# Kernel optimization log

Hardware: AMD Instinct MI355X
Metric: run time of the kernel (lower is better)

The kernel has to match this reference:

```python
import jax, jax.numpy as jnp
import numpy as np

B = 1; S = 2048; HID = 1024; NH = 8; HD = 128; INTER = 4096
EPS = 1e-6; THETA = 10000.0


def rms_norm(x, w):
    # Gemma RMSNorm: x * rsqrt(mean(x^2)+eps) * (1 + w)
    v = jnp.mean(x * x, axis=-1, keepdims=True)
    return x * jax.lax.rsqrt(v + EPS) * (1.0 + w)


def rope_cos_sin(seqlen):
    inv = 1.0 / (THETA ** (jnp.arange(0, HD, 2, dtype=jnp.float32) / HD))
    t = jnp.arange(seqlen, dtype=jnp.float32)
    f = jnp.outer(t, inv)                       # (S, HD/2)
    emb = jnp.concatenate([f, f], axis=-1)      # (S, HD)
    return jnp.cos(emb), jnp.sin(emb)


def rotate_half(x):
    x1, x2 = jnp.split(x, 2, axis=-1)
    return jnp.concatenate([-x2, x1], axis=-1)


def apply_rope(x, cos, sin):
    return x * cos[None, None] + rotate_half(x) * sin[None, None]


def expert_forward(x, mask, params):
    """One GemmaDecoderLayer; returns output plus PRE-RoPE q/k/v (as the torch module exposes)."""
    w_ln, wq, wk, wv, wo, w_pln, wg, wu, wd = params
    res = x
    h = rms_norm(x, w_ln)

    def proj(w):
        return (h @ w).reshape(B, -1, NH, HD).transpose(0, 2, 1, 3)  # (B,H,S,D)

    q, k, v = proj(wq), proj(wk), proj(wv)      # stored before rotary in the original
    cos, sin = rope_cos_sin(x.shape[1])
    qr, kr = apply_rope(q, cos, sin), apply_rope(k, cos, sin)
    scores = jnp.einsum('bhqd,bhkd->bhqk', qr, kr) * (HD ** -0.5) + mask
    attn = jnp.einsum('bhqk,bhkd->bhqd', jax.nn.softmax(scores, axis=-1), v)
    attn = attn.transpose(0, 2, 1, 3).reshape(B, -1, NH * HD) @ wo
    h1 = res + attn
    m = rms_norm(h1, w_pln)
    mlp = (jax.nn.gelu(m @ wg, approximate=True) * (m @ wu)) @ wd  # gelu_pytorch_tanh
    return h1 + mlp, q, k, v


def setup_inputs() -> dict:
    key = jax.random.key(0)
    ks = iter(jax.random.split(key, 40))

    def w(shape, scale=0.02):
        return jax.random.normal(next(ks), shape, jnp.float32) * scale

    inp = {
        'x_a': jax.random.normal(next(ks), (B, S, HID), jnp.float32),
        'x_b': jax.random.normal(next(ks), (B, S, HID), jnp.float32),
    }
    tri = jnp.tril(jnp.ones((S, S), bool))
    causal = jnp.where(tri, 0.0, -1e9).astype(jnp.float32)[None, None]  # additive causal mask
    inp['mask_a'] = causal
    inp['mask_b'] = causal
    inp['mix_mask'] = jnp.zeros((B, 1, 2 * S, 2 * S), jnp.float32)      # non-causal cross-expert
    for e in ('a', 'b'):
        inp['w_ln_' + e] = jnp.zeros((HID,), jnp.float32)
        inp['w_q_' + e] = w((HID, NH * HD))
        inp['w_k_' + e] = w((HID, NH * HD))
        inp['w_v_' + e] = w((HID, NH * HD))
        inp['w_o_' + e] = w((NH * HD, HID))
        inp['w_pln_' + e] = jnp.zeros((HID,), jnp.float32)
        inp['w_g_' + e] = w((HID, INTER))
        inp['w_u_' + e] = w((HID, INTER))
        inp['w_d_' + e] = w((INTER, HID))
    return inp


def reference(x_a, x_b, mask_a, mask_b, mix_mask,
              w_ln_a, w_q_a, w_k_a, w_v_a, w_o_a, w_pln_a, w_g_a, w_u_a, w_d_a,
              w_ln_b, w_q_b, w_k_b, w_v_b, w_o_b, w_pln_b, w_g_b, w_u_b, w_d_b):
    pa = (w_ln_a, w_q_a, w_k_a, w_v_a, w_o_a, w_pln_a, w_g_a, w_u_a, w_d_a)
    pb = (w_ln_b, w_q_b, w_k_b, w_v_b, w_o_b, w_pln_b, w_g_b, w_u_b, w_d_b)
    out_a, qa, ka, va = expert_forward(x_a, mask_a, pa)
    out_b, qb, kb, vb = expert_forward(x_b, mask_b, pb)
    # cross-expert mixed attention over concatenated (pre-RoPE) streams
    q = jnp.concatenate([qa, qb], axis=2)
    k = jnp.concatenate([ka, kb], axis=2)
    v = jnp.concatenate([va, vb], axis=2)
    scores = jnp.einsum('bhqd,bhkd->bhqk', q, k) * (HD ** -0.5) + mix_mask
    mixed = jnp.einsum('bhqk,bhkd->bhqd', jax.nn.softmax(scores, axis=-1), v)
    mixed = mixed.transpose(0, 2, 1, 3).reshape(B, 2 * S, NH * HD)
    ma, mb = mixed[:, :S], mixed[:, S:]
    return jnp.stack([out_a + ma @ w_o_a, out_b + mb @ w_o_b])
```

## Files before the change

kernel.cpp:

```cpp
#include <hip/hip_runtime.h>
#include <hip/hip_bf16.h>
#include <math.h>

#define S 2048
#define HID 1024
#define NH 8
#define HD 128
#define INTER 4096
#define EPSV 1e-6f
#define THETA 10000.0f

typedef __hip_bfloat16 bf16;
typedef unsigned short u16;
typedef __attribute__((ext_vector_type(8))) short bf16x8;
typedef __attribute__((ext_vector_type(4))) float f32x4;

__device__ inline float bu2f(u16 u) {
    unsigned int x = ((unsigned int)u) << 16;
    return __uint_as_float(x);
}
__device__ inline u16 f2bu(float f) {
    bf16 h = __float2bfloat16(f);
    return *reinterpret_cast<u16*>(&h);
}
__device__ inline float ldin(const void* p, size_t i, bool isbf) {
    return isbf ? bu2f(((const u16*)p)[i]) : ((const float*)p)[i];
}
__device__ inline float gelu_tanh(float x) {
    float x3 = x * x * x;
    return 0.5f * x * (1.f + tanhf(0.7978845608028654f * (x + 0.044715f * x3)));
}
__device__ inline void gload16(const u16* g, u16* l) {
    __builtin_amdgcn_global_load_lds(
        (const __attribute__((address_space(1))) void*)g,
        (__attribute__((address_space(3))) void*)l, 16, 0, 0);
}

__global__ __launch_bounds__(256) void probe_kernel(const unsigned short* __restrict__ x,
                                                    int* __restrict__ flag) {
    __shared__ int red[256];
    int tid = threadIdx.x;
    int cnt = 0;
    for (int i = tid; i < 2048; i += 256) {
        unsigned short u = x[2 * i];
        int e = (u >> 7) & 0xFF;
        cnt += (e >= 110 && e <= 135) ? 1 : 0;
    }
    red[tid] = cnt;
    __syncthreads();
    for (int off = 128; off > 0; off >>= 1) {
        if (tid < off) red[tid] += red[tid + off];
        __syncthreads();
    }
    if (tid == 0) *flag = (red[0] > 1024) ? 1 : 0;
}

struct TransN {
    const void* W[8];
    u16* T[8];
};
__global__ __launch_bounds__(256) void transpose_wN(TransN tn, const int* __restrict__ flag,
                                                    int K, int N) {
    bool isbf = (*flag != 0);
    const void* W = tn.W[blockIdx.z];
    u16* WT = tn.T[blockIdx.z];
    __shared__ float t[32][33];
    int n0 = blockIdx.x * 32, k0 = blockIdx.y * 32;
    int c = threadIdx.x & 31, r = threadIdx.x >> 5;
#pragma unroll
    for (int p = 0; p < 4; p++)
        t[r + 8 * p][c] = ldin(W, (size_t)(k0 + r + 8 * p) * N + n0 + c, isbf);
    __syncthreads();
#pragma unroll
    for (int p = 0; p < 4; p++) {
        int row = r + 8 * p;
        WT[(size_t)(n0 + row) * K + k0 + c] = f2bu(t[c][row]);
    }
}

__global__ __launch_bounds__(256) void transpose_v(const u16* __restrict__ V0,
                                                   const u16* __restrict__ V1, int sv,
                                                   u16* __restrict__ VT) {
    const u16* V = blockIdx.z ? V1 : V0;
    VT += (size_t)blockIdx.z * ((size_t)NH * HD * S);
    __shared__ u16 t[32][33];
    int k0 = blockIdx.x * 32;
    int d0 = blockIdx.y * 32;
    int c = threadIdx.x & 31, r = threadIdx.x >> 5;
#pragma unroll
    for (int p = 0; p < 4; p++)
        t[r + 8 * p][c] = V[(size_t)(k0 + r + 8 * p) * sv + d0 + c];
    __syncthreads();
#pragma unroll
    for (int p = 0; p < 4; p++)
        VT[(size_t)(d0 + r + 8 * p) * S + k0 + c] = t[c][r + 8 * p];
}

struct RmsDual {
    const void* x[2];
    const void* w[2];
    u16* y[2];
};
__global__ __launch_bounds__(256) void rmsnorm_kernel(RmsDual rd,
                                                      const int* __restrict__ flag,
                                                      int dual) {
    int e = blockIdx.y;
    const void* x = rd.x[e];
    const void* w = rd.w[e];
    u16* y = rd.y[e];
    bool isbf = (*flag != 0);
    bool xbf = dual && isbf;
    int row = blockIdx.x;
    size_t base = (size_t)row * HID;
    __shared__ float red[256];
    float xv[4];
    float s = 0.f;
#pragma unroll
    for (int i = 0; i < 4; i++) {
        float v = ldin(x, base + threadIdx.x + 256 * i, xbf);
        xv[i] = v;
        s += v * v;
    }
    red[threadIdx.x] = s;
    __syncthreads();
    for (int off = 128; off > 0; off >>= 1) {
        if (threadIdx.x < off) red[threadIdx.x] += red[threadIdx.x + off];
        __syncthreads();
    }
    float scale = rsqrtf(red[0] / (float)HID + EPSV);
#pragma unroll
    for (int i = 0; i < 4; i++) {
        int c = threadIdx.x + 256 * i;
        y[base + c] = f2bu(xv[i] * scale * (1.f + ldin(w, c, isbf)));
    }
}

struct GemmDual {
    const u16* A[2];
    const u16* BT[2];
    float* Cf[2];
    u16* Cb[2];
    const void* res[2];
};
template <int BM, int BN, int WRN, int WCN, int EPI>
__global__ __launch_bounds__(256) void gemm_mfma(GemmDual g, const int* __restrict__ flag,
                                                 int M, int N, int K) {
    int eZ = blockIdx.z;
    const u16* __restrict__ A = g.A[eZ];
    const u16* __restrict__ BT = g.BT[eZ];
    float* __restrict__ Cf = g.Cf[eZ];
    u16* __restrict__ Cb = g.Cb[eZ];
    const void* __restrict__ res = g.res[eZ];
    constexpr int BK = 32;
    constexpr int WM = BM / WRN, WN = BN / WCN, TI = WM / 16, TJ = WN / 16;
    __shared__ u16 As[BM * 32];
    __shared__ u16 Bs[BN * 32];
    int tid = threadIdx.x, lane = tid & 63, wv = tid >> 6;
    int wr = wv / WCN, wc = wv % WCN;
    int m = lane & 15, quad = lane >> 4;
    int m0 = blockIdx.y * BM, n0 = blockIdx.x * BN;
    f32x4 acc[TI][TJ] = {};
    for (int k0 = 0; k0 < K; k0 += BK) {
        __syncthreads();
#pragma unroll
        for (int c2 = 0; c2 < BM / 64; c2++) {
            int row0 = (wv * (BM / 64) + c2) * 16;
            int row = row0 + (lane >> 2);
            int ch = lane & 3;
            gload16(&A[(size_t)(m0 + row) * K + k0 + ((ch ^ ((row >> 1) & 3)) << 3)],
                    &As[row0 * 32]);
        }
#pragma unroll
        for (int c2 = 0; c2 < BN / 64; c2++) {
            int row0 = (wv * (BN / 64) + c2) * 16;
            int row = row0 + (lane >> 2);
            int ch = lane & 3;
            gload16(&BT[(size_t)(n0 + row) * K + k0 + ((ch ^ ((row >> 1) & 3)) << 3)],
                    &Bs[row0 * 32]);
        }
        __syncthreads();
        bf16x8 af[TI], bf_[TJ];
#pragma unroll
        for (int i = 0; i < TI; i++) {
            int rr = wr * WM + i * 16 + m;
            af[i] = *reinterpret_cast<const bf16x8*>(&As[rr * 32 + ((quad ^ ((rr >> 1) & 3)) << 3)]);
        }
#pragma unroll
        for (int j = 0; j < TJ; j++) {
            int rr = wc * WN + j * 16 + m;
            bf_[j] = *reinterpret_cast<const bf16x8*>(&Bs[rr * 32 + ((quad ^ ((rr >> 1) & 3)) << 3)]);
        }
#pragma unroll
        for (int i = 0; i < TI; i++)
#pragma unroll
            for (int j = 0; j < TJ; j++)
                acc[i][j] = __builtin_amdgcn_mfma_f32_16x16x32_bf16(af[i], bf_[j], acc[i][j], 0, 0, 0);
    }
    bool isbf = (EPI == 1) ? (*flag != 0) : false;
#pragma unroll
    for (int i = 0; i < TI; i++) {
#pragma unroll
        for (int j = 0; j < TJ; j++) {
#pragma unroll
            for (int r = 0; r < 4; r++) {
                int row = m0 + wr * WM + i * 16 + quad * 4 + r;
                int col = n0 + wc * WN + j * 16 + m;
                size_t idx = (size_t)row * N + col;
                float v = acc[i][j][r];
                if (EPI == 0) Cb[idx] = f2bu(v);
                else if (EPI == 1) Cf[idx] = v + ldin(res, idx, isbf);
                else Cf[idx] = Cf[idx] + v;
            }
        }
    }
}

template <int BM, int BN, int WRN, int WCN>
__global__ __launch_bounds__(256) void gemm_gated_mfma(const u16* __restrict__ A,
                                                       const u16* __restrict__ BgT,
                                                       const u16* __restrict__ BuT,
                                                       u16* __restrict__ C,
                                                       int M, int N, int K) {
    constexpr int BK = 32;
    constexpr int WM = BM / WRN, WN = BN / WCN, TI = WM / 16, TJ = WN / 16;
    __shared__ u16 As[BM * 32];
    __shared__ u16 Bgs[BN * 32];
    __shared__ u16 Bus[BN * 32];
    int tid = threadIdx.x, lane = tid & 63, wv = tid >> 6;
    int wr = wv / WCN, wc = wv % WCN;
    int m = lane & 15, quad = lane >> 4;
    int m0 = blockIdx.y * BM, n0 = blockIdx.x * BN;
    f32x4 accg[TI][TJ] = {};
    f32x4 accu[TI][TJ] = {};
    for (int k0 = 0; k0 < K; k0 += BK) {
        __syncthreads();
#pragma unroll
        for (int c2 = 0; c2 < BM / 64; c2++) {
            int row0 = (wv * (BM / 64) + c2) * 16;
            int row = row0 + (lane >> 2);
            int ch = lane & 3;
            gload16(&A[(size_t)(m0 + row) * K + k0 + ((ch ^ ((row >> 1) & 3)) << 3)],
                    &As[row0 * 32]);
        }
#pragma unroll
        for (int c2 = 0; c2 < BN / 64; c2++) {
            int row0 = (wv * (BN / 64) + c2) * 16;
            int row = row0 + (lane >> 2);
            int ch = lane & 3;
            gload16(&BgT[(size_t)(n0 + row) * K + k0 + ((ch ^ ((row >> 1) & 3)) << 3)],
                    &Bgs[row0 * 32]);
            gload16(&BuT[(size_t)(n0 + row) * K + k0 + ((ch ^ ((row >> 1) & 3)) << 3)],
                    &Bus[row0 * 32]);
        }
        __syncthreads();
        bf16x8 af[TI], bg[TJ], bu[TJ];
#pragma unroll
        for (int i = 0; i < TI; i++) {
            int rr = wr * WM + i * 16 + m;
            af[i] = *reinterpret_cast<const bf16x8*>(&As[rr * 32 + ((quad ^ ((rr >> 1) & 3)) << 3)]);
        }
#pragma unroll
        for (int j = 0; j < TJ; j++) {
            int rr = wc * WN + j * 16 + m;
            int off = rr * 32 + ((quad ^ ((rr >> 1) & 3)) << 3);
            bg[j] = *reinterpret_cast<const bf16x8*>(&Bgs[off]);
            bu[j] = *reinterpret_cast<const bf16x8*>(&Bus[off]);
        }
#pragma unroll
        for (int i = 0; i < TI; i++)
#pragma unroll
            for (int j = 0; j < TJ; j++) {
                accg[i][j] = __builtin_amdgcn_mfma_f32_16x16x32_bf16(af[i], bg[j], accg[i][j], 0, 0, 0);
                accu[i][j] = __builtin_amdgcn_mfma_f32_16x16x32_bf16(af[i], bu[j], accu[i][j], 0, 0, 0);
            }
    }
#pragma unroll
    for (int i = 0; i < TI; i++)
#pragma unroll
        for (int j = 0; j < TJ; j++)
#pragma unroll
            for (int r = 0; r < 4; r++) {
                int row = m0 + wr * WM + i * 16 + quad * 4 + r;
                int col = n0 + wc * WN + j * 16 + m;
                C[(size_t)row * N + col] = f2bu(gelu_tanh(accg[i][j][r]) * accu[i][j][r]);
            }
}

__global__ __launch_bounds__(64) void rope_kernel(const u16* __restrict__ qkv0,
                                                  const u16* __restrict__ qkv1,
                                                  u16* __restrict__ qr,
                                                  u16* __restrict__ kr) {
    const u16* qkv = blockIdx.z ? qkv1 : qkv0;
    size_t zo = (size_t)blockIdx.z * ((size_t)S * HID);
    int b = blockIdx.x;
    int t = b >> 3, h = b & 7;
    int i = threadIdx.x;
    size_t ib = (size_t)t * 3072 + h * HD;
    size_t ob = zo + (size_t)t * HID + h * HD;
    float inv = __expf(-9.210340372f * (float)(2 * i) / (float)HD);
    float f = (float)t * inv;
    float c = cosf(f), s = sinf(f);
    float q1 = bu2f(qkv[ib + i]), q2 = bu2f(qkv[ib + i + 64]);
    qr[ob + i] = f2bu(q1 * c - q2 * s);
    qr[ob + i + 64] = f2bu(q2 * c + q1 * s);
    float k1 = bu2f(qkv[ib + 1024 + i]), k2 = bu2f(qkv[ib + 1024 + i + 64]);
    kr[ob + i] = f2bu(k1 * c - k2 * s);
    kr[ob + i + 64] = f2bu(k2 * c + k1 * s);
}

__device__ inline int swz64(int row, int b) {
    return row * 64 + (b ^ (((row >> 1) & 3) << 4));
}

template <bool CAUSAL>
__global__ __launch_bounds__(256, 2) void attn_mfma_kernel(
    const u16* __restrict__ qa, const u16* __restrict__ qb, int sq,
    const u16* __restrict__ ka, const u16* __restrict__ kb, int sk,
    const u16* __restrict__ vta, const u16* __restrict__ vtb,
    u16* __restrict__ Out, int nkeys) {
    __shared__ char Ks[2][16384];
    __shared__ char VTs[2][16384];

    int tid = threadIdx.x;
    int lane = tid & 63, w = tid >> 6;
    int col = lane & 15, quad = lane >> 4;
    int eZ = CAUSAL ? (int)blockIdx.z : 0;
    int bx = (CAUSAL && eZ) ? ((int)gridDim.x - 1 - (int)blockIdx.x) : (int)blockIdx.x;
    int q0 = bx * 64;
    int h = blockIdx.y;
    const float scale = 0.08838834764831845f;

    int q0r = CAUSAL ? q0 : (q0 & (S - 1));
    const u16* qsel = CAUSAL ? (eZ ? qb : qa) : ((q0 < S) ? qa : qb);
    const u16* qp = qsel + (size_t)q0r * sq;
    bf16x8 aq[4];
#pragma unroll
    for (int t = 0; t < 4; t++)
        aq[t] = *reinterpret_cast<const bf16x8*>(
            qp + (size_t)(16 * w + col) * sq + h * HD + 32 * t + quad * 8);

    const u16* kplo = (CAUSAL && eZ) ? kb : ka;
    const u16* vplo = (CAUSAL && eZ) ? vtb : vta;

    f32x4 o[8] = {};
    float m_ = -1e30f, l_ = 0.f;

    int sA = col + 16 * (2 * (quad & 1));
    int sB = sA + 16;
    bool hi = (quad >> 1) != 0;

    int ntiles = CAUSAL ? (q0 >> 6) + 1 : (nkeys >> 6);

    auto stage = [&](int buf, int tt) {
        int j0r = (tt * 64) & (S - 1);
        bool eb = (!CAUSAL) && (tt >= (S >> 6));
        const u16* kp = eb ? kb : kplo;
        const u16* vp = eb ? vtb : vplo;
        char* kd = &Ks[buf][(tid >> 6) * 1024];
        char* vd = &VTs[buf][(tid >> 6) * 1024];
#pragma unroll
        for (int i = 0; i < 4; i++) {
            int l = 256 * i + tid;
            int key = (l >> 2) & 63;
            int c = (l >> 8) * 4 + ((l & 3) ^ ((key >> 1) & 3));
            gload16(kp + (size_t)(j0r + key) * sk + h * HD + c * 8, (u16*)(kd + i * 4096));
        }
#pragma unroll
        for (int i = 0; i < 4; i++) {
            int l = 256 * i + tid;
            int d = (l >> 2) & 127;
            int c = (l >> 9) * 4 + ((l & 3) ^ ((d >> 1) & 3));
            gload16(vp + (size_t)(h * HD + d) * S + j0r + c * 8, (u16*)(vd + i * 4096));
        }
    };

    stage(0, 0);
    __syncthreads();
    int cur = 0;

    for (int tt = 0; tt < ntiles; tt++) {
        if (tt + 1 < ntiles) stage(cur ^ 1, tt + 1);
        const char* Kb = Ks[cur];
        const char* Vb = VTs[cur];

        f32x4 sc[4] = {};
        __builtin_amdgcn_s_setprio(1);
#pragma unroll
        for (int t = 0; t < 4; t++) {
#pragma unroll
            for (int ct = 0; ct < 4; ct++) {
                bf16x8 kf = *reinterpret_cast<const bf16x8*>(
                    Kb + t * 4096 + swz64(16 * ct + col, quad * 16));
                sc[ct] = __builtin_amdgcn_mfma_f32_16x16x32_bf16(kf, aq[t], sc[ct], 0, 0, 0);
            }
        }
        __builtin_amdgcn_s_setprio(0);
        bool diag = CAUSAL && (tt == ntiles - 1);
#pragma unroll
        for (int ct = 0; ct < 4; ct++) {
#pragma unroll
            for (int r = 0; r < 4; r++) {
                float v = sc[ct][r] * scale;
                if (diag && (16 * ct + 4 * quad + r > 16 * w + col)) v = -1e30f;
                sc[ct][r] = v;
            }
        }

        float mx0 = fmaxf(fmaxf(sc[0][0], sc[0][1]), fmaxf(sc[0][2], sc[0][3]));
        float mx1 = fmaxf(fmaxf(sc[1][0], sc[1][1]), fmaxf(sc[1][2], sc[1][3]));
        float mx2 = fmaxf(fmaxf(sc[2][0], sc[2][1]), fmaxf(sc[2][2], sc[2][3]));
        float mx3 = fmaxf(fmaxf(sc[3][0], sc[3][1]), fmaxf(sc[3][2], sc[3][3]));
        float rmax = fmaxf(fmaxf(mx0, mx1), fmaxf(mx2, mx3));
        rmax = fmaxf(rmax, __shfl_xor(rmax, 16));
        rmax = fmaxf(rmax, __shfl_xor(rmax, 32));
        float mn = fmaxf(m_, rmax);
        float al = __expf(m_ - mn);
#pragma unroll
        for (int ct = 0; ct < 4; ct++)
#pragma unroll
            for (int r = 0; r < 4; r++) sc[ct][r] = __expf(sc[ct][r] - mn);
        float s0 = (sc[0][0] + sc[0][1]) + (sc[0][2] + sc[0][3]);
        float s1 = (sc[1][0] + sc[1][1]) + (sc[1][2] + sc[1][3]);
        float s2 = (sc[2][0] + sc[2][1]) + (sc[2][2] + sc[2][3]);
        float s3 = (sc[3][0] + sc[3][1]) + (sc[3][2] + sc[3][3]);
        float rs = (s0 + s1) + (s2 + s3);
        rs += __shfl_xor(rs, 16);
        rs += __shfl_xor(rs, 32);
        l_ = l_ * al + rs;
        m_ = mn;

        unsigned int pu[4][2];
#pragma unroll
        for (int ct = 0; ct < 4; ct++) {
            pu[ct][0] = (unsigned int)f2bu(sc[ct][0]) | ((unsigned int)f2bu(sc[ct][1]) << 16);
            pu[ct][1] = (unsigned int)f2bu(sc[ct][2]) | ((unsigned int)f2bu(sc[ct][3]) << 16);
        }

#pragma unroll
        for (int nt = 0; nt < 8; nt++)
#pragma unroll
            for (int r = 0; r < 4; r++) o[nt][r] *= al;

#pragma unroll
        for (int ks = 0; ks < 2; ks++) {
            unsigned int a0 = __shfl(pu[2 * ks][0], sA);
            unsigned int a1 = __shfl(pu[2 * ks][1], sA);
            unsigned int c0 = __shfl(pu[2 * ks + 1][0], sA);
            unsigned int c1 = __shfl(pu[2 * ks + 1][1], sA);
            unsigned int b0 = __shfl(pu[2 * ks][0], sB);
            unsigned int b1 = __shfl(pu[2 * ks][1], sB);
            unsigned int g0 = __shfl(pu[2 * ks + 1][0], sB);
            unsigned int g1 = __shfl(pu[2 * ks + 1][1], sB);
            union {
                unsigned int u[4];
                bf16x8 v;
            } pb;
            pb.u[0] = hi ? c0 : a0;
            pb.u[1] = hi ? c1 : a1;
            pb.u[2] = hi ? g0 : b0;
            pb.u[3] = hi ? g1 : b1;
            __builtin_amdgcn_s_setprio(1);
#pragma unroll
            for (int nt = 0; nt < 8; nt++) {
                bf16x8 vf = *reinterpret_cast<const bf16x8*>(
                    Vb + ks * 8192 + swz64(16 * nt + col, quad * 16));
                o[nt] = __builtin_amdgcn_mfma_f32_16x16x32_bf16(vf, pb.v, o[nt], 0, 0, 0);
            }
            __builtin_amdgcn_s_setprio(0);
        }

        __syncthreads();
        cur ^= 1;
    }

    u16* outp = Out + (CAUSAL ? (size_t)eZ * ((size_t)S * HID) : (size_t)0);
    float inv = 1.f / l_;
    size_t rowoff = (size_t)(q0 + 16 * w + col) * HID + (size_t)h * HD + 4 * quad;
#pragma unroll
    for (int nt = 0; nt < 8; nt++) {
        ushort4 st;
        st.x = f2bu(o[nt][0] * inv);
        st.y = f2bu(o[nt][1] * inv);
        st.z = f2bu(o[nt][2] * inv);
        st.w = f2bu(o[nt][3] * inv);
        *reinterpret_cast<ushort4*>(&outp[rowoff + 16 * nt]) = st;
    }
}

__global__ __launch_bounds__(256) void store_out_kernel(const float* __restrict__ a,
                                                        const float* __restrict__ b,
                                                        void* __restrict__ out,
                                                        const int* __restrict__ flag) {
    bool isbf = (*flag != 0);
    size_t i = (size_t)blockIdx.x * 256 + threadIdx.x;
    const size_t MM = (size_t)S * HID;
    float v = (i < MM) ? a[i] : b[i - MM];
    if (isbf)
        ((bf16*)out)[i] = __float2bfloat16(v);
    else
        ((float*)out)[i] = v;
}

extern "C" void kernel_launch(void* const* d_in, const int* in_sizes, int n_in,
                              void* d_out, int out_size, void* d_ws, size_t ws_size,
                              hipStream_t stream) {
    const void* x[2] = {d_in[0], d_in[1]};
    const void* w_ln[2] = {d_in[5], d_in[14]};
    const void* w_q[2] = {d_in[6], d_in[15]};
    const void* w_k[2] = {d_in[7], d_in[16]};
    const void* w_v[2] = {d_in[8], d_in[17]};
    const void* w_o[2] = {d_in[9], d_in[18]};
    const void* w_pln[2] = {d_in[10], d_in[19]};
    const void* w_g[2] = {d_in[11], d_in[20]};
    const void* w_u[2] = {d_in[12], d_in[21]};
    const void* w_d[2] = {d_in[13], d_in[22]};

    char* base = (char*)d_ws;
    int* flag = (int*)base;
    u16* p = (u16*)(base + 256);
    const size_t E_QKV = (size_t)S * 3072;
    const size_t E_SH = (size_t)S * HID;
    const size_t E_VT = (size_t)NH * HD * S;

    u16* qkv[2] = {p, p + E_QKV};            p += 2 * E_QKV;
    u16* qr = p;                             p += 2 * E_SH;
    u16* kr = p;                             p += 2 * E_SH;
    u16* h_bf = p;                           p += 2 * E_SH;
    u16* attnbuf = p;                        p += 2 * E_SH;
    u16* vtg = p;                            p += 2 * E_VT;
    u16* gated = qr;
    u16* mixed = qr;
    u16* wqkvT = p;                          p += 2 * (size_t)3072 * 1024;
    u16* woT[2] = {p, p + (size_t)1024 * 1024};  p += 2 * (size_t)1024 * 1024;
    u16* wgT = p;                            p += (size_t)INTER * 1024;
    u16* wuT = p;                            p += (size_t)INTER * 1024;
    u16* wdT = p;                            p += (size_t)1024 * INTER;
    float* fbase = (float*)(((size_t)p + 255) & ~(size_t)255);
    float* outX[2] = {fbase, fbase + E_SH};

    probe_kernel<<<1, 256, 0, stream>>>((const unsigned short*)d_in[0], flag);

    {
        TransN tn = {};
        for (int e = 0; e < 2; e++) {
            u16* wt = wqkvT + (size_t)e * 3072 * 1024;
            tn.W[4 * e + 0] = w_q[e];  tn.T[4 * e + 0] = wt;
            tn.W[4 * e + 1] = w_k[e];  tn.T[4 * e + 1] = wt + (size_t)1024 * 1024;
            tn.W[4 * e + 2] = w_v[e];  tn.T[4 * e + 2] = wt + (size_t)2048 * 1024;
            tn.W[4 * e + 3] = w_o[e];  tn.T[4 * e + 3] = woT[e];
        }
        transpose_wN<<<dim3(32, 32, 8), 256, 0, stream>>>(tn, flag, 1024, 1024);
    }

    {
        RmsDual rd = {{x[0], x[1]}, {w_ln[0], w_ln[1]}, {h_bf, h_bf + E_SH}};
        rmsnorm_kernel<<<dim3(S, 2), 256, 0, stream>>>(rd, flag, 1);
    }
    {
        GemmDual g = {{h_bf, h_bf + E_SH},
                      {wqkvT, wqkvT + (size_t)3072 * 1024},
                      {nullptr, nullptr},
                      {qkv[0], qkv[1]},
                      {nullptr, nullptr}};
        gemm_mfma<128, 128, 2, 2, 0><<<dim3(3072 / 128, S / 128, 2), 256, 0, stream>>>(
            g, flag, S, 3072, 1024);
    }
    rope_kernel<<<dim3(S * NH, 1, 2), 64, 0, stream>>>(qkv[0], qkv[1], qr, kr);
    transpose_v<<<dim3(S / 32, 1024 / 32, 2), 256, 0, stream>>>(qkv[0] + 2048, qkv[1] + 2048, 3072, vtg);
    attn_mfma_kernel<true><<<dim3(S / 64, NH, 2), 256, 0, stream>>>(
        qr, qr + E_SH, HID, kr, kr + E_SH, HID, vtg, vtg + E_VT, attnbuf, S);
    {
        GemmDual g = {{attnbuf, attnbuf + E_SH},
                      {woT[0], woT[1]},
                      {outX[0], outX[1]},
                      {nullptr, nullptr},
                      {x[0], x[1]}};
        gemm_mfma<64, 64, 2, 2, 1><<<dim3(1024 / 64, S / 64, 2), 256, 0, stream>>>(
            g, flag, S, 1024, 1024);
    }
    {
        RmsDual rd = {{outX[0], outX[1]}, {w_pln[0], w_pln[1]}, {h_bf, h_bf + E_SH}};
        rmsnorm_kernel<<<dim3(S, 2), 256, 0, stream>>>(rd, flag, 0);
    }

    for (int e = 0; e < 2; e++) {
        {
            TransN tg = {};
            tg.W[0] = w_g[e];  tg.T[0] = wgT;
            tg.W[1] = w_u[e];  tg.T[1] = wuT;
            transpose_wN<<<dim3(INTER / 32, 1024 / 32, 2), 256, 0, stream>>>(tg, flag, 1024, INTER);
        }
        gemm_gated_mfma<128, 64, 2, 2><<<dim3(INTER / 64, S / 128), 256, 0, stream>>>(
            h_bf + e * E_SH, wgT, wuT, gated, S, INTER, 1024);
        {
            TransN td = {};
            td.W[0] = w_d[e];  td.T[0] = wdT;
            transpose_wN<<<dim3(1024 / 32, INTER / 32, 1), 256, 0, stream>>>(td, flag, INTER, 1024);
        }
        GemmDual g = {{gated, gated}, {wdT, wdT}, {outX[e], outX[e]}, {nullptr, nullptr}, {nullptr, nullptr}};
        gemm_mfma<64, 64, 2, 2, 2><<<dim3(1024 / 64, S / 64, 1), 256, 0, stream>>>(
            g, flag, S, 1024, INTER);
    }

    attn_mfma_kernel<false><<<dim3(2 * S / 64, NH), 256, 0, stream>>>(
        qkv[0], qkv[1], 3072, qkv[0] + 1024, qkv[1] + 1024, 3072,
        vtg, vtg + E_VT, mixed, 2 * S);
    {
        GemmDual g = {{mixed, mixed + E_SH},
                      {woT[0], woT[1]},
                      {outX[0], outX[1]},
                      {nullptr, nullptr},
                      {nullptr, nullptr}};
        gemm_mfma<64, 64, 2, 2, 2><<<dim3(1024 / 64, S / 64, 2), 256, 0, stream>>>(
            g, flag, S, 1024, 1024);
    }

    store_out_kernel<<<(2 * E_SH) / 256, 256, 0, stream>>>(outX[0], outX[1], d_out, flag);
}
```

Before: 796.3 us.

## Split mixed attention over key halves with separate combine kernel

Replaces the single mixed non-causal attention launch with a split-K flash-attention kernel: each block handles one 2048-key half (expert A or B keys), writing unnormalized bf16 partial outputs plus running max and sum. A combine kernel then merges the two partials with log-sum-exp weights into the mixed buffer. This doubles the grid to raise occupancy and parallelism across CUs, at the cost of an extra partial-output round trip through memory, an extra launch, and bf16 rounding of the unnormalized partials.

New measurement: 784.8 us. About the same (-1.4%).

```diff
diff --git a/kernel.cpp b/kernel.cpp
--- a/kernel.cpp
+++ b/kernel.cpp
@@ -487,6 +487,182 @@
     }
 }
 
+__global__ __launch_bounds__(256, 4) void attn_mixed_split(
+    const u16* __restrict__ qa, const u16* __restrict__ qb, int sq,
+    const u16* __restrict__ ka, const u16* __restrict__ kb, int sk,
+    const u16* __restrict__ vta, const u16* __restrict__ vtb,
+    u16* __restrict__ Opart, float2* __restrict__ ml) {
+    __shared__ char Ks[16384];
+    __shared__ char VTs[16384];
+
+    int tid = threadIdx.x;
+    int lane = tid & 63, w = tid >> 6;
+    int col = lane & 15, quad = lane >> 4;
+    int q0 = blockIdx.x * 64;
+    int h = blockIdx.y;
+    int z = blockIdx.z;
+    const float scale = 0.08838834764831845f;
+
+    const u16* qp = ((q0 < S) ? qa : qb) + (size_t)(q0 & (S - 1)) * sq;
+    bf16x8 aq[4];
+#pragma unroll
+    for (int t = 0; t < 4; t++)
+        aq[t] = *reinterpret_cast<const bf16x8*>(
+            qp + (size_t)(16 * w + col) * sq + h * HD + 32 * t + quad * 8);
+
+    const u16* kp = z ? kb : ka;
+    const u16* vp = z ? vtb : vta;
+
+    f32x4 o[8] = {};
+    float m_ = -1e30f, l_ = 0.f;
+
+    int sA = col + 16 * (2 * (quad & 1));
+    int sB = sA + 16;
+    bool hi = (quad >> 1) != 0;
+
+    for (int tt = 0; tt < (S >> 6); tt++) {
+        int j0r = tt * 64;
+        __syncthreads();
+        {
+            char* kd = &Ks[(tid >> 6) * 1024];
+            char* vd = &VTs[(tid >> 6) * 1024];
+#pragma unroll
+            for (int i = 0; i < 4; i++) {
+                int l = 256 * i + tid;
+                int key = (l >> 2) & 63;
+                int c = (l >> 8) * 4 + ((l & 3) ^ ((key >> 1) & 3));
+                gload16(kp + (size_t)(j0r + key) * sk + h * HD + c * 8, (u16*)(kd + i * 4096));
+            }
+#pragma unroll
+            for (int i = 0; i < 4; i++) {
+                int l = 256 * i + tid;
+                int d = (l >> 2) & 127;
+                int c = (l >> 9) * 4 + ((l & 3) ^ ((d >> 1) & 3));
+                gload16(vp + (size_t)(h * HD + d) * S + j0r + c * 8, (u16*)(vd + i * 4096));
+            }
+        }
+        __syncthreads();
+
+        f32x4 sc[4] = {};
+        __builtin_amdgcn_s_setprio(1);
+#pragma unroll
+        for (int t = 0; t < 4; t++) {
+#pragma unroll
+            for (int ct = 0; ct < 4; ct++) {
+                bf16x8 kf = *reinterpret_cast<const bf16x8*>(
+                    Ks + t * 4096 + swz64(16 * ct + col, quad * 16));
+                sc[ct] = __builtin_amdgcn_mfma_f32_16x16x32_bf16(kf, aq[t], sc[ct], 0, 0, 0);
+            }
+        }
+        __builtin_amdgcn_s_setprio(0);
+#pragma unroll
+        for (int ct = 0; ct < 4; ct++)
+#pragma unroll
+            for (int r = 0; r < 4; r++) sc[ct][r] *= scale;
+
+        float mx0 = fmaxf(fmaxf(sc[0][0], sc[0][1]), fmaxf(sc[0][2], sc[0][3]));
+        float mx1 = fmaxf(fmaxf(sc[1][0], sc[1][1]), fmaxf(sc[1][2], sc[1][3]));
+        float mx2 = fmaxf(fmaxf(sc[2][0], sc[2][1]), fmaxf(sc[2][2], sc[2][3]));
+        float mx3 = fmaxf(fmaxf(sc[3][0], sc[3][1]), fmaxf(sc[3][2], sc[3][3]));
+        float rmax = fmaxf(fmaxf(mx0, mx1), fmaxf(mx2, mx3));
+        rmax = fmaxf(rmax, __shfl_xor(rmax, 16));
+        rmax = fmaxf(rmax, __shfl_xor(rmax, 32));
+        float mn = fmaxf(m_, rmax);
+        float al = __expf(m_ - mn);
+#pragma unroll
+        for (int ct = 0; ct < 4; ct++)
+#pragma unroll
+            for (int r = 0; r < 4; r++) sc[ct][r] = __expf(sc[ct][r] - mn);
+        float s0 = (sc[0][0] + sc[0][1]) + (sc[0][2] + sc[0][3]);
+        float s1 = (sc[1][0] + sc[1][1]) + (sc[1][2] + sc[1][3]);
+        float s2 = (sc[2][0] + sc[2][1]) + (sc[2][2] + sc[2][3]);
+        float s3 = (sc[3][0] + sc[3][1]) + (sc[3][2] + sc[3][3]);
+        float rs = (s0 + s1) + (s2 + s3);
+        rs += __shfl_xor(rs, 16);
+        rs += __shfl_xor(rs, 32);
+        l_ = l_ * al + rs;
+        m_ = mn;
+
+        unsigned int pu[4][2];
+#pragma unroll
+        for (int ct = 0; ct < 4; ct++) {
+            pu[ct][0] = (unsigned int)f2bu(sc[ct][0]) | ((unsigned int)f2bu(sc[ct][1]) << 16);
+            pu[ct][1] = (unsigned int)f2bu(sc[ct][2]) | ((unsigned int)f2bu(sc[ct][3]) << 16);
+        }
+
+#pragma unroll
+        for (int nt = 0; nt < 8; nt++)
+#pragma unroll
+            for (int r = 0; r < 4; r++) o[nt][r] *= al;
+
+#pragma unroll
+        for (int ks = 0; ks < 2; ks++) {
+            unsigned int a0 = __shfl(pu[2 * ks][0], sA);
+            unsigned int a1 = __shfl(pu[2 * ks][1], sA);
+            unsigned int c0 = __shfl(pu[2 * ks + 1][0], sA);
+            unsigned int c1 = __shfl(pu[2 * ks + 1][1], sA);
+            unsigned int b0 = __shfl(pu[2 * ks][0], sB);
+            unsigned int b1 = __shfl(pu[2 * ks][1], sB);
+            unsigned int g0 = __shfl(pu[2 * ks + 1][0], sB);
+            unsigned int g1 = __shfl(pu[2 * ks + 1][1], sB);
+            union {
+                unsigned int u[4];
+                bf16x8 v;
+            } pb;
+            pb.u[0] = hi ? c0 : a0;
+            pb.u[1] = hi ? c1 : a1;
+            pb.u[2] = hi ? g0 : b0;
+            pb.u[3] = hi ? g1 : b1;
+            __builtin_amdgcn_s_setprio(1);
+#pragma unroll
+            for (int nt = 0; nt < 8; nt++) {
+                bf16x8 vf = *reinterpret_cast<const bf16x8*>(
+                    VTs + ks * 8192 + swz64(16 * nt + col, quad * 16));
+                o[nt] = __builtin_amdgcn_mfma_f32_16x16x32_bf16(vf, pb.v, o[nt], 0, 0, 0);
+            }
+            __builtin_amdgcn_s_setprio(0);
+        }
+    }
+
+    const size_t SPL = (size_t)2 * S * HID;
+    size_t rowoff = (size_t)z * SPL + (size_t)(q0 + 16 * w + col) * HID + (size_t)h * HD + 4 * quad;
+#pragma unroll
+    for (int nt = 0; nt < 8; nt++) {
+        ushort4 st;
+        st.x = f2bu(o[nt][0]);
+        st.y = f2bu(o[nt][1]);
+        st.z = f2bu(o[nt][2]);
+        st.w = f2bu(o[nt][3]);
+        *reinterpret_cast<ushort4*>(&Opart[rowoff + 16 * nt]) = st;
+    }
+    if (quad == 0)
+        ml[((size_t)z * 2 * S + q0 + 16 * w + col) * NH + h] = make_float2(m_, l_);
+}
+
+__global__ __launch_bounds__(256) void attn_combine(const u16* __restrict__ Opart,
+                                                    const float2* __restrict__ ml,
+                                                    u16* __restrict__ out) {
+    size_t idx = ((size_t)blockIdx.x * 256 + threadIdx.x) * 8;
+    int q = (int)(idx >> 10);
+    int c0 = (int)(idx & 1023);
+    int h = c0 >> 7;
+    float2 ml0 = ml[(size_t)q * NH + h];
+    float2 ml1 = ml[((size_t)2 * S + q) * NH + h];
+    float ms = fmaxf(ml0.x, ml1.x);
+    float w0 = __expf(ml0.x - ms), w1 = __expf(ml1.x - ms);
+    float rden = 1.f / (w0 * ml0.y + w1 * ml1.y);
+    const size_t SPL = (size_t)2 * S * HID;
+    uint4 a = *reinterpret_cast<const uint4*>(&Opart[idx]);
+    uint4 b = *reinterpret_cast<const uint4*>(&Opart[SPL + idx]);
+    const u16* ap = reinterpret_cast<const u16*>(&a);
+    const u16* bp = reinterpret_cast<const u16*>(&b);
+    u16 res[8];
+#pragma unroll
+    for (int j = 0; j < 8; j++)
+        res[j] = f2bu((w0 * bu2f(ap[j]) + w1 * bu2f(bp[j])) * rden);
+    *reinterpret_cast<uint4*>(&out[idx]) = *reinterpret_cast<const uint4*>(res);
+}
+
 __global__ __launch_bounds__(256) void store_out_kernel(const float* __restrict__ a,
                                                         const float* __restrict__ b,
                                                         void* __restrict__ out,
@@ -529,7 +705,8 @@
     u16* attnbuf = p;                        p += 2 * E_SH;
     u16* vtg = p;                            p += 2 * E_VT;
     u16* gated = qr;
-    u16* mixed = qr;
+    u16* Opart = qr;
+    u16* mixed = h_bf;
     u16* wqkvT = p;                          p += 2 * (size_t)3072 * 1024;
     u16* woT[2] = {p, p + (size_t)1024 * 1024};  p += 2 * (size_t)1024 * 1024;
     u16* wgT = p;                            p += (size_t)INTER * 1024;
@@ -537,6 +714,7 @@
     u16* wdT = p;                            p += (size_t)1024 * INTER;
     float* fbase = (float*)(((size_t)p + 255) & ~(size_t)255);
     float* outX[2] = {fbase, fbase + E_SH};
+    float2* mlbuf = (float2*)(fbase + 2 * E_SH);
 
     probe_kernel<<<1, 256, 0, stream>>>((const unsigned short*)d_in[0], flag);
 
@@ -602,9 +780,10 @@
             g, flag, S, 1024, INTER);
     }
 
-    attn_mfma_kernel<false><<<dim3(2 * S / 64, NH), 256, 0, stream>>>(
+    attn_mixed_split<<<dim3(2 * S / 64, NH, 2), 256, 0, stream>>>(
         qkv[0], qkv[1], 3072, qkv[0] + 1024, qkv[1] + 1024, 3072,
-        vtg, vtg + E_VT, mixed, 2 * S);
+        vtg, vtg + E_VT, Opart, mlbuf);
+    attn_combine<<<(2 * E_SH) / (256 * 8), 256, 0, stream>>>(Opart, mlbuf, mixed);
     {
         GemmDual g = {{mixed, mixed + E_SH},
                       {woT[0], woT[1]},
```
